# Kernel tuning notes

Measured on AMD Instinct MI355X. Metric: run time of the kernel, lower is better.

## Reference

```python
import jax, jax.numpy as jnp
import numpy as np

N, E, IN, H, D = 50000, 800000, 128, 4, 32
NEG_SLOPE = 0.2


def setup_inputs() -> dict:
    key = jax.random.key(0)
    ks = jax.random.split(key, 7)
    feat = jax.random.normal(ks[0], (N, IN), dtype=jnp.float32)
    src = jax.random.randint(ks[1], (E,), 0, N)
    dst = jax.random.randint(ks[2], (E,), 0, N)
    fc_w = jax.random.normal(ks[3], (H * D, IN), dtype=jnp.float32) * 0.05
    attn_l = jax.random.normal(ks[4], (H, D), dtype=jnp.float32) * 0.05
    attn_r = jax.random.normal(ks[5], (H, D), dtype=jnp.float32) * 0.05
    res_w = jax.random.normal(ks[6], (H * D, IN), dtype=jnp.float32) * 0.05
    return {"feat": feat, "src": src, "dst": dst, "fc_w": fc_w,
            "attn_l": attn_l, "attn_r": attn_r, "res_w": res_w}


def reference(feat, src, dst, fc_w, attn_l, attn_r, res_w):
    # Shared linear projection: [N, H, D]
    h = (feat @ fc_w.T).reshape(N, H, D)
    # Per-node attention logits: el (source side), er (destination side), [N, H]
    el = jnp.einsum("nhd,hd->nh", h, attn_l)
    er = jnp.einsum("nhd,hd->nh", h, attn_r)
    # Per-edge score and exp (original uses plain exp, no max-subtraction)
    e = jax.nn.leaky_relu(el[src] + er[dst], negative_slope=NEG_SLOPE)  # [E, H]
    coeff = jnp.exp(e)
    # Softmax denominator per destination node
    denom = jax.ops.segment_sum(coeff, dst, num_segments=N)  # [N, H]
    alpha = coeff / denom[dst]  # [E, H]
    # Weighted aggregation of source features into destinations: [N, H, D]
    msg = alpha[:, :, None] * h[src]  # [E, H, D]
    rst = jax.ops.segment_sum(msg, dst, num_segments=N)
    # Residual projection (always applied in this module)
    resval = (feat @ res_w.T).reshape(N, H, D)
    return rst + resval
```

## Files before the change

kernel.cpp:

```cpp
#include <hip/hip_runtime.h>
#include <hip/hip_bf16.h>

#define NN 50000
#define EE 800000
#define HH 4
#define HDIM 128
#define CAP 64

#define GEMM_BLOCKS ((NN + 63) / 64)
#define CHUNKS      (EE / 4)
#define GRP_BLOCKS  ((CHUNKS + 255) / 256)
#define ZERO_BLOCKS ((NN + 255) / 256)
#define W16_BLOCKS  16

typedef __attribute__((ext_vector_type(8))) short bf16x8;
typedef __attribute__((ext_vector_type(4))) float f32x4;

__device__ inline unsigned short f2bf(float f) {
    unsigned u = __float_as_uint(f);
    u = u + 0x7FFFu + ((u >> 16) & 1u);
    return (unsigned short)(u >> 16);
}
__device__ inline float bfl(unsigned u) { return __uint_as_float(u << 16); }
__device__ inline float bfh(unsigned u) { return __uint_as_float(u & 0xFFFF0000u); }

__global__ void prep_kernel(int* __restrict__ cnt,
                            const float* __restrict__ fc_w,
                            const float* __restrict__ res_w,
                            unsigned short* __restrict__ w16) {
    int bx = blockIdx.x;
    int t = threadIdx.x;
    if (bx < ZERO_BLOCKS) {
        int idx = bx * 256 + t;
        if (idx < NN) cnt[idx] = 0;
    } else {
        int idx = (bx - ZERO_BLOCKS) * 256 + t;
        int base = idx * 8;
        if (base < 256 * 128) {
            const float* sw = (base < 128 * 128) ? &fc_w[base] : &res_w[base - 128 * 128];
            float4 v0 = *(const float4*)&sw[0];
            float4 v1 = *(const float4*)&sw[4];
            unsigned short tmp[8] = { f2bf(v0.x), f2bf(v0.y), f2bf(v0.z), f2bf(v0.w),
                                      f2bf(v1.x), f2bf(v1.y), f2bf(v1.z), f2bf(v1.w) };
            *(uint4*)&w16[base] = *(uint4*)tmp;
        }
    }
}

__global__ void scatter_kernel(const int* __restrict__ src,
                               const int* __restrict__ dst,
                               int* __restrict__ cnt,
                               int* __restrict__ perm_src) {
    int g = blockIdx.x & 7;
    int cidx = (blockIdx.x >> 3) * 256 + threadIdx.x;
    int e4 = cidx * 4;
    if (e4 >= EE) return;
    int4 s4 = *(const int4*)&src[e4];
    int4 d4 = *(const int4*)&dst[e4];
    if ((d4.x & 7) == g) {
        int p = atomicAdd(&cnt[d4.x], 1);
        if (p < CAP) perm_src[d4.x * CAP + p] = s4.x;
    }
    if ((d4.y & 7) == g) {
        int p = atomicAdd(&cnt[d4.y], 1);
        if (p < CAP) perm_src[d4.y * CAP + p] = s4.y;
    }
    if ((d4.z & 7) == g) {
        int p = atomicAdd(&cnt[d4.z], 1);
        if (p < CAP) perm_src[d4.z * CAP + p] = s4.z;
    }
    if ((d4.w & 7) == g) {
        int p = atomicAdd(&cnt[d4.w], 1);
        if (p < CAP) perm_src[d4.w * CAP + p] = s4.w;
    }
}

__global__ __launch_bounds__(256) void gemm_elr_kernel(const float* __restrict__ feat,
                                                       const unsigned short* __restrict__ w16,
                                                       const float* __restrict__ al,
                                                       const float* __restrict__ ar,
                                                       unsigned short* __restrict__ h16,
                                                       float* __restrict__ el,
                                                       float* __restrict__ er,
                                                       float* __restrict__ out,
                                                       int n) {
    __shared__ unsigned short As[64][136];
    __shared__ unsigned short Hs[64][136];
    int t = threadIdx.x;
    int w = t >> 6;
    int l = t & 63;
    int l15 = l & 15;
    int kg = l >> 4;
    int r0 = blockIdx.x * 64;
    int colbase = w * 64;

    bf16x8 bfrag[4][4];
    #pragma unroll
    for (int ct = 0; ct < 4; ++ct) {
        int col = colbase + ct * 16 + l15;
        #pragma unroll
        for (int ks = 0; ks < 4; ++ks)
            bfrag[ct][ks] = *(const bf16x8*)&w16[(size_t)col * 128 + ks * 32 + kg * 8];
    }

    for (int i = t; i < 64 * 32; i += 256) {
        int r = i >> 5;
        int c4 = (i & 31) << 2;
        float4 v = make_float4(0.f, 0.f, 0.f, 0.f);
        if (r0 + r < n) v = *(const float4*)&feat[(size_t)(r0 + r) * 128 + c4];
        unsigned short tmp[4] = { f2bf(v.x), f2bf(v.y), f2bf(v.z), f2bf(v.w) };
        *(uint2*)&As[r][c4] = *(uint2*)tmp;
    }
    __syncthreads();

    f32x4 acc[4][4];
    #pragma unroll
    for (int rt = 0; rt < 4; ++rt)
        #pragma unroll
        for (int ct = 0; ct < 4; ++ct)
            acc[rt][ct] = (f32x4){0.f, 0.f, 0.f, 0.f};

    #pragma unroll
    for (int ks = 0; ks < 4; ++ks) {
        bf16x8 afrag[4];
        #pragma unroll
        for (int rt = 0; rt < 4; ++rt)
            afrag[rt] = *(const bf16x8*)&As[rt * 16 + l15][ks * 32 + kg * 8];
        #pragma unroll
        for (int rt = 0; rt < 4; ++rt)
            #pragma unroll
            for (int ct = 0; ct < 4; ++ct)
                acc[rt][ct] = __builtin_amdgcn_mfma_f32_16x16x32_bf16(
                    afrag[rt], bfrag[ct][ks], acc[rt][ct], 0, 0, 0);
    }

    int rb = 4 * kg;
    if (w < 2) {
        #pragma unroll
        for (int rt = 0; rt < 4; ++rt)
            #pragma unroll
            for (int ct = 0; ct < 4; ++ct)
                #pragma unroll
                for (int r = 0; r < 4; ++r)
                    Hs[rt * 16 + rb + r][colbase + ct * 16 + l15] = f2bf(acc[rt][ct][r]);
    } else {
        #pragma unroll
        for (int rt = 0; rt < 4; ++rt)
            #pragma unroll
            for (int ct = 0; ct < 4; ++ct)
                #pragma unroll
                for (int r = 0; r < 4; ++r) {
                    int row = r0 + rt * 16 + rb + r;
                    if (row < n)
                        out[(size_t)row * 128 + (colbase - 128) + ct * 16 + l15] = acc[rt][ct][r];
                }
    }
    __syncthreads();

    #pragma unroll
    for (int it = 0; it < 4; ++it) {
        int flat = it * 2048 + t * 8;
        int row = flat >> 7;
        int col = flat & 127;
        if (r0 + row < n)
            *(uint4*)&h16[(size_t)(r0 + row) * 128 + col] = *(const uint4*)&Hs[row][col];
    }

    int node = t >> 2;
    int hh = t & 3;
    if (r0 + node < n) {
        const unsigned short* hp = &Hs[node][hh * 32];
        const float* alp = &al[hh * 32];
        const float* arp = &ar[hh * 32];
        float a = 0.f, b = 0.f;
        #pragma unroll
        for (int c = 0; c < 4; ++c) {
            uint4 hv = *(const uint4*)&hp[c * 8];
            unsigned uu[4] = { hv.x, hv.y, hv.z, hv.w };
            #pragma unroll
            for (int j = 0; j < 4; ++j) {
                float v0 = bfl(uu[j]);
                float v1 = bfh(uu[j]);
                int d = c * 8 + j * 2;
                a = fmaf(v0, alp[d], a);     a = fmaf(v1, alp[d + 1], a);
                b = fmaf(v0, arp[d], b);     b = fmaf(v1, arp[d + 1], b);
            }
        }
        el[(size_t)(r0 + node) * 4 + hh] = a;
        er[(size_t)(r0 + node) * 4 + hh] = b;
    }
}

__global__ __launch_bounds__(256) void gather_agg_kernel(const int* __restrict__ cnt,
                                                         const int* __restrict__ perm_src,
                                                         const float* __restrict__ el,
                                                         const float* __restrict__ er,
                                                         const unsigned short* __restrict__ h16,
                                                         float* __restrict__ out) {
    __shared__ int   Ss[8][CAP];
    __shared__ float Cs[8][CAP][HH];
    int t = threadIdx.x;
    int nl = t >> 5;
    int node = blockIdx.x * 8 + nl;
    int ln = t & 31;
    int d0 = ln << 2;
    int hh = ln >> 3;
    int q  = ln & 7;
    int deg = cnt[node];
    if (deg > CAP) deg = CAP;
    int o0 = node * CAP;
    float erh = er[node * 4 + hh];

    float dsum = 0.f;
    for (int j = q; j < deg; j += 8) {
        int s = perm_src[o0 + j];
        if (hh == 0) Ss[nl][j] = s;
        float x = el[s * 4 + hh] + erh;
        x = (x > 0.f) ? x : 0.2f * x;
        float c = __expf(x);
        Cs[nl][j][hh] = c;
        dsum += c;
    }
    dsum += __shfl_xor(dsum, 1, 64);
    dsum += __shfl_xor(dsum, 2, 64);
    dsum += __shfl_xor(dsum, 4, 64);
    float inv = (deg > 0) ? 1.0f / dsum : 0.f;
    __syncthreads();

    float4 acc = make_float4(0.f, 0.f, 0.f, 0.f);
    int j = 0;
    for (; j + 3 < deg; j += 4) {
        int s0 = Ss[nl][j];
        int s1 = Ss[nl][j + 1];
        int s2 = Ss[nl][j + 2];
        int s3 = Ss[nl][j + 3];
        float c0 = Cs[nl][j][hh];
        float c1 = Cs[nl][j + 1][hh];
        float c2 = Cs[nl][j + 2][hh];
        float c3 = Cs[nl][j + 3][hh];
        uint2 h0 = *(const uint2*)&h16[(size_t)s0 * 128 + d0];
        uint2 h1 = *(const uint2*)&h16[(size_t)s1 * 128 + d0];
        uint2 h2 = *(const uint2*)&h16[(size_t)s2 * 128 + d0];
        uint2 h3 = *(const uint2*)&h16[(size_t)s3 * 128 + d0];
        acc.x = fmaf(c0, bfl(h0.x), acc.x); acc.y = fmaf(c0, bfh(h0.x), acc.y);
        acc.z = fmaf(c0, bfl(h0.y), acc.z); acc.w = fmaf(c0, bfh(h0.y), acc.w);
        acc.x = fmaf(c1, bfl(h1.x), acc.x); acc.y = fmaf(c1, bfh(h1.x), acc.y);
        acc.z = fmaf(c1, bfl(h1.y), acc.z); acc.w = fmaf(c1, bfh(h1.y), acc.w);
        acc.x = fmaf(c2, bfl(h2.x), acc.x); acc.y = fmaf(c2, bfh(h2.x), acc.y);
        acc.z = fmaf(c2, bfl(h2.y), acc.z); acc.w = fmaf(c2, bfh(h2.y), acc.w);
        acc.x = fmaf(c3, bfl(h3.x), acc.x); acc.y = fmaf(c3, bfh(h3.x), acc.y);
        acc.z = fmaf(c3, bfl(h3.y), acc.z); acc.w = fmaf(c3, bfh(h3.y), acc.w);
    }
    for (; j < deg; ++j) {
        int s0 = Ss[nl][j];
        float c0 = Cs[nl][j][hh];
        uint2 h0 = *(const uint2*)&h16[(size_t)s0 * 128 + d0];
        acc.x = fmaf(c0, bfl(h0.x), acc.x); acc.y = fmaf(c0, bfh(h0.x), acc.y);
        acc.z = fmaf(c0, bfl(h0.y), acc.z); acc.w = fmaf(c0, bfh(h0.y), acc.w);
    }
    size_t oidx = (size_t)node * 128 + d0;
    float4 res = *(const float4*)&out[oidx];
    res.x = fmaf(acc.x, inv, res.x);
    res.y = fmaf(acc.y, inv, res.y);
    res.z = fmaf(acc.z, inv, res.z);
    res.w = fmaf(acc.w, inv, res.w);
    *(float4*)&out[oidx] = res;
}

extern "C" void kernel_launch(void* const* d_in, const int* in_sizes, int n_in,
                              void* d_out, int out_size, void* d_ws, size_t ws_size,
                              hipStream_t stream) {
    const float* feat   = (const float*)d_in[0];
    const int*   src    = (const int*)d_in[1];
    const int*   dst    = (const int*)d_in[2];
    const float* fc_w   = (const float*)d_in[3];
    const float* attn_l = (const float*)d_in[4];
    const float* attn_r = (const float*)d_in[5];
    const float* res_w  = (const float*)d_in[6];
    float* out = (float*)d_out;

    unsigned short* h16 = (unsigned short*)d_ws;
    float* el  = (float*)(h16 + (size_t)NN * HDIM);
    float* er  = el + (size_t)NN * HH;
    unsigned short* w16 = (unsigned short*)(er + (size_t)NN * HH);
    int*   perm_src = (int*)(w16 + 256 * 128);
    int*   cnt      = perm_src + (size_t)NN * CAP;

    prep_kernel<<<ZERO_BLOCKS + W16_BLOCKS, 256, 0, stream>>>(cnt, fc_w, res_w, w16);

    scatter_kernel<<<8 * GRP_BLOCKS, 256, 0, stream>>>(src, dst, cnt, perm_src);

    gemm_elr_kernel<<<GEMM_BLOCKS, 256, 0, stream>>>(feat, w16, attn_l, attn_r,
                                                     h16, el, er, out, NN);

    gather_agg_kernel<<<NN / 8, 256, 0, stream>>>(cnt, perm_src, el, er, h16, out);
}
```

Baseline: 117.2 us.

## Store residual as bf16 staging, move weight conversion into scatter, unroll gather by 8

The GEMM kernel now writes the residual projection to a bf16 workspace buffer through shared memory instead of writing fp32 directly to the output. The gather kernel then reads that bf16 residual and writes the output once, removing an fp32 write plus read-modify-write of the output. The weight-to-bf16 conversion moves from the zeroing kernel into extra blocks of the scatter kernel, and the gather loop is unrolled by 8 to keep more independent loads in flight. The residual is rounded to bf16, which costs some precision, and an extra __syncthreads is added so As can be reused.

```diff
diff --git a/kernel.cpp b/kernel.cpp
--- a/kernel.cpp
+++ b/kernel.cpp
@@ -24,17 +24,20 @@
 __device__ inline float bfl(unsigned u) { return __uint_as_float(u << 16); }
 __device__ inline float bfh(unsigned u) { return __uint_as_float(u & 0xFFFF0000u); }
 
-__global__ void prep_kernel(int* __restrict__ cnt,
-                            const float* __restrict__ fc_w,
-                            const float* __restrict__ res_w,
-                            unsigned short* __restrict__ w16) {
-    int bx = blockIdx.x;
-    int t = threadIdx.x;
-    if (bx < ZERO_BLOCKS) {
-        int idx = bx * 256 + t;
-        if (idx < NN) cnt[idx] = 0;
-    } else {
-        int idx = (bx - ZERO_BLOCKS) * 256 + t;
+__global__ void zero_kernel(int* __restrict__ cnt) {
+    int idx = blockIdx.x * 256 + threadIdx.x;
+    if (idx < NN) cnt[idx] = 0;
+}
+
+__global__ void scatter_kernel(const int* __restrict__ src,
+                               const int* __restrict__ dst,
+                               int* __restrict__ cnt,
+                               int* __restrict__ perm_src,
+                               const float* __restrict__ fc_w,
+                               const float* __restrict__ res_w,
+                               unsigned short* __restrict__ w16) {
+    if (blockIdx.x >= 8 * GRP_BLOCKS) {
+        int idx = (blockIdx.x - 8 * GRP_BLOCKS) * 256 + threadIdx.x;
         int base = idx * 8;
         if (base < 256 * 128) {
             const float* sw = (base < 128 * 128) ? &fc_w[base] : &res_w[base - 128 * 128];
@@ -44,13 +47,8 @@
                                       f2bf(v1.x), f2bf(v1.y), f2bf(v1.z), f2bf(v1.w) };
             *(uint4*)&w16[base] = *(uint4*)tmp;
         }
-    }
-}
-
-__global__ void scatter_kernel(const int* __restrict__ src,
-                               const int* __restrict__ dst,
-                               int* __restrict__ cnt,
-                               int* __restrict__ perm_src) {
+        return;
+    }
     int g = blockIdx.x & 7;
     int cidx = (blockIdx.x >> 3) * 256 + threadIdx.x;
     int e4 = cidx * 4;
@@ -80,9 +78,9 @@
                                                        const float* __restrict__ al,
                                                        const float* __restrict__ ar,
                                                        unsigned short* __restrict__ h16,
+                                                       unsigned short* __restrict__ res16,
                                                        float* __restrict__ el,
                                                        float* __restrict__ er,
-                                                       float* __restrict__ out,
                                                        int n) {
     __shared__ unsigned short As[64][136];
     __shared__ unsigned short Hs[64][136];
@@ -133,6 +131,7 @@
                 acc[rt][ct] = __builtin_amdgcn_mfma_f32_16x16x32_bf16(
                     afrag[rt], bfrag[ct][ks], acc[rt][ct], 0, 0, 0);
     }
+    __syncthreads();
 
     int rb = 4 * kg;
     if (w < 2) {
@@ -149,11 +148,8 @@
             #pragma unroll
             for (int ct = 0; ct < 4; ++ct)
                 #pragma unroll
-                for (int r = 0; r < 4; ++r) {
-                    int row = r0 + rt * 16 + rb + r;
-                    if (row < n)
-                        out[(size_t)row * 128 + (colbase - 128) + ct * 16 + l15] = acc[rt][ct][r];
-                }
+                for (int r = 0; r < 4; ++r)
+                    As[rt * 16 + rb + r][(colbase - 128) + ct * 16 + l15] = f2bf(acc[rt][ct][r]);
     }
     __syncthreads();
 
@@ -162,8 +158,10 @@
         int flat = it * 2048 + t * 8;
         int row = flat >> 7;
         int col = flat & 127;
-        if (r0 + row < n)
+        if (r0 + row < n) {
             *(uint4*)&h16[(size_t)(r0 + row) * 128 + col] = *(const uint4*)&Hs[row][col];
+            *(uint4*)&res16[(size_t)(r0 + row) * 128 + col] = *(const uint4*)&As[row][col];
+        }
     }
 
     int node = t >> 2;
@@ -196,6 +194,7 @@
                                                          const float* __restrict__ el,
                                                          const float* __restrict__ er,
                                                          const unsigned short* __restrict__ h16,
+                                                         const unsigned short* __restrict__ res16,
                                                          float* __restrict__ out) {
     __shared__ int   Ss[8][CAP];
     __shared__ float Cs[8][CAP][HH];
@@ -229,27 +228,39 @@
 
     float4 acc = make_float4(0.f, 0.f, 0.f, 0.f);
     int j = 0;
+    for (; j + 7 < deg; j += 8) {
+        uint2 hv[8];
+        float cc[8];
+        #pragma unroll
+        for (int k = 0; k < 8; ++k) {
+            int s = Ss[nl][j + k];
+            cc[k] = Cs[nl][j + k][hh];
+            hv[k] = *(const uint2*)&h16[(size_t)s * 128 + d0];
+        }
+        #pragma unroll
+        for (int k = 0; k < 8; ++k) {
+            acc.x = fmaf(cc[k], bfl(hv[k].x), acc.x);
+            acc.y = fmaf(cc[k], bfh(hv[k].x), acc.y);
+            acc.z = fmaf(cc[k], bfl(hv[k].y), acc.z);
+            acc.w = fmaf(cc[k], bfh(hv[k].y), acc.w);
+        }
+    }
     for (; j + 3 < deg; j += 4) {
-        int s0 = Ss[nl][j];
-        int s1 = Ss[nl][j + 1];
-        int s2 = Ss[nl][j + 2];
-        int s3 = Ss[nl][j + 3];
-        float c0 = Cs[nl][j][hh];
-        float c1 = Cs[nl][j + 1][hh];
-        float c2 = Cs[nl][j + 2][hh];
-        float c3 = Cs[nl][j + 3][hh];
-        uint2 h0 = *(const uint2*)&h16[(size_t)s0 * 128 + d0];
-        uint2 h1 = *(const uint2*)&h16[(size_t)s1 * 128 + d0];
-        uint2 h2 = *(const uint2*)&h16[(size_t)s2 * 128 + d0];
-        uint2 h3 = *(const uint2*)&h16[(size_t)s3 * 128 + d0];
-        acc.x = fmaf(c0, bfl(h0.x), acc.x); acc.y = fmaf(c0, bfh(h0.x), acc.y);
-        acc.z = fmaf(c0, bfl(h0.y), acc.z); acc.w = fmaf(c0, bfh(h0.y), acc.w);
-        acc.x = fmaf(c1, bfl(h1.x), acc.x); acc.y = fmaf(c1, bfh(h1.x), acc.y);
-        acc.z = fmaf(c1, bfl(h1.y), acc.z); acc.w = fmaf(c1, bfh(h1.y), acc.w);
-        acc.x = fmaf(c2, bfl(h2.x), acc.x); acc.y = fmaf(c2, bfh(h2.x), acc.y);
-        acc.z = fmaf(c2, bfl(h2.y), acc.z); acc.w = fmaf(c2, bfh(h2.y), acc.w);
-        acc.x = fmaf(c3, bfl(h3.x), acc.x); acc.y = fmaf(c3, bfh(h3.x), acc.y);
-        acc.z = fmaf(c3, bfl(h3.y), acc.z); acc.w = fmaf(c3, bfh(h3.y), acc.w);
+        uint2 hv[4];
+        float cc[4];
+        #pragma unroll
+        for (int k = 0; k < 4; ++k) {
+            int s = Ss[nl][j + k];
+            cc[k] = Cs[nl][j + k][hh];
+            hv[k] = *(const uint2*)&h16[(size_t)s * 128 + d0];
+        }
+        #pragma unroll
+        for (int k = 0; k < 4; ++k) {
+            acc.x = fmaf(cc[k], bfl(hv[k].x), acc.x);
+            acc.y = fmaf(cc[k], bfh(hv[k].x), acc.y);
+            acc.z = fmaf(cc[k], bfl(hv[k].y), acc.z);
+            acc.w = fmaf(cc[k], bfh(hv[k].y), acc.w);
+        }
     }
     for (; j < deg; ++j) {
         int s0 = Ss[nl][j];
@@ -259,11 +270,12 @@
         acc.z = fmaf(c0, bfl(h0.y), acc.z); acc.w = fmaf(c0, bfh(h0.y), acc.w);
     }
     size_t oidx = (size_t)node * 128 + d0;
-    float4 res = *(const float4*)&out[oidx];
-    res.x = fmaf(acc.x, inv, res.x);
-    res.y = fmaf(acc.y, inv, res.y);
-    res.z = fmaf(acc.z, inv, res.z);
-    res.w = fmaf(acc.w, inv, res.w);
+    uint2 rv = *(const uint2*)&res16[oidx];
+    float4 res;
+    res.x = fmaf(acc.x, inv, bfl(rv.x));
+    res.y = fmaf(acc.y, inv, bfh(rv.x));
+    res.z = fmaf(acc.z, inv, bfl(rv.y));
+    res.w = fmaf(acc.w, inv, bfh(rv.y));
     *(float4*)&out[oidx] = res;
 }
 
@@ -279,19 +291,21 @@
     const float* res_w  = (const float*)d_in[6];
     float* out = (float*)d_out;
 
-    unsigned short* h16 = (unsigned short*)d_ws;
-    float* el  = (float*)(h16 + (size_t)NN * HDIM);
+    unsigned short* h16   = (unsigned short*)d_ws;
+    unsigned short* res16 = h16 + (size_t)NN * HDIM;
+    float* el  = (float*)(res16 + (size_t)NN * HDIM);
     float* er  = el + (size_t)NN * HH;
     unsigned short* w16 = (unsigned short*)(er + (size_t)NN * HH);
     int*   perm_src = (int*)(w16 + 256 * 128);
     int*   cnt      = perm_src + (size_t)NN * CAP;
 
-    prep_kernel<<<ZERO_BLOCKS + W16_BLOCKS, 256, 0, stream>>>(cnt, fc_w, res_w, w16);
-
-    scatter_kernel<<<8 * GRP_BLOCKS, 256, 0, stream>>>(src, dst, cnt, perm_src);
+    zero_kernel<<<ZERO_BLOCKS, 256, 0, stream>>>(cnt);
+
+    scatter_kernel<<<8 * GRP_BLOCKS + W16_BLOCKS, 256, 0, stream>>>(
+        src, dst, cnt, perm_src, fc_w, res_w, w16);
 
     gemm_elr_kernel<<<GEMM_BLOCKS, 256, 0, stream>>>(feat, w16, attn_l, attn_r,
-                                                     h16, el, er, out, NN);
-
-    gather_agg_kernel<<<NN / 8, 256, 0, stream>>>(cnt, perm_src, el, er, h16, out);
-}
+                                                     h16, res16, el, er, NN);
+
+    gather_agg_kernel<<<NN / 8, 256, 0, stream>>>(cnt, perm_src, el, er, h16, res16, out);
+}
```

New measurement: 113.8 us. 2.9% less time.
